# Kernel optimization log

Hardware: AMD Instinct MI355X
Metric: run time of the kernel (lower is better)

The kernel has to match this reference:

```python
import jax, jax.numpy as jnp
import numpy as np

B, S, D = 4, 2048, 512
H, DK, DV = 8, 64, 64
DFF = 2048
LN_EPS = 1e-5


def _layernorm(x, g, b):
    mu = jnp.mean(x, axis=-1, keepdims=True)
    var = jnp.mean(jnp.square(x - mu), axis=-1, keepdims=True)
    return (x - mu) * jax.lax.rsqrt(var + LN_EPS) * g + b


def setup_inputs() -> dict:
    key = jax.random.key(0)
    ks = jax.random.split(key, 9)
    def xavier(k, shape):
        fan_out, fan_in = shape
        std = np.sqrt(2.0 / (fan_in + fan_out))
        return jax.random.normal(k, shape, jnp.float32) * std
    GELU_GAIN = 1.85
    return {
        "x": jax.random.normal(ks[0], (B, S, D), jnp.float32),
        "attention_mask": jax.random.randint(ks[1], (B, S), 0, 2).astype(bool),
        "Wq": xavier(ks[2], (H * DK, D)),
        "Wk": xavier(ks[3], (H * DK, D)),
        "Wv": xavier(ks[4], (H * DV, D)),
        "Wp": xavier(ks[5], (D, H * DV)),
        "W1": xavier(ks[6], (DFF, D)) * GELU_GAIN,
        "b1": jnp.zeros((DFF,), jnp.float32),
        "W2": xavier(ks[7], (D, DFF)),
        "b2": jnp.zeros((D,), jnp.float32),
        "ln1_g": jnp.ones((D,), jnp.float32),
        "ln1_b": jnp.zeros((D,), jnp.float32),
        "ln2_g": jnp.ones((D,), jnp.float32),
        "ln2_b": jnp.zeros((D,), jnp.float32),
    }


def reference(x, attention_mask, Wq, Wk, Wv, Wp, W1, b1, W2, b2,
              ln1_g, ln1_b, ln2_g, ln2_b):
    b, s, d = x.shape
    residual = x
    q = (x @ Wq.T).reshape(b, s, H, DK)  # [B,S,H,DK]
    k = (x @ Wk.T).reshape(b, s, H, DK)
    v = (x @ Wv.T).reshape(b, s, H, DV)
    score = jnp.einsum("bshd,bthd->bhst", q, k) * (DK ** -0.5)  # [B,H,S,S]
    # subtractive mask: score -= 100 * not(mask)
    score = score - 100.0 * (~attention_mask)[:, None, None, :].astype(score.dtype)
    p = jax.nn.softmax(score, axis=-1)
    ctx = jnp.einsum("bhst,bthd->bshd", p, v).reshape(b, s, H * DV)
    att = ctx @ Wp.T  # dropout p=0.1 is identity in eval
    h = _layernorm(att + residual, ln1_g, ln1_b)
    ff = jax.nn.gelu(h @ W1.T + b1, approximate=False) @ W2.T + b2
    out = _layernorm(ff + h, ln2_g, ln2_b)
    return out
```

## Files before the change

### kernel.cpp

```cpp
#include <hip/hip_runtime.h>
#include <cstdint>
#include <cstddef>

#define B_ 4
#define S_ 2048
#define D_ 512
#define H_ 8
#define DK_ 64
#define DFF_ 2048

using s16x8  = __attribute__((ext_vector_type(8))) short;
using bf16x8 = __attribute__((ext_vector_type(8))) __bf16;
using f32x4  = __attribute__((ext_vector_type(4))) float;

__device__ __forceinline__ short f2bf(float f) {
  unsigned u = __builtin_bit_cast(unsigned, f);
  u += 0x7FFFu + ((u >> 16) & 1u);
  return (short)(u >> 16);
}
__device__ __forceinline__ float bf2f(short s) {
  unsigned u = ((unsigned)(unsigned short)s) << 16;
  return __builtin_bit_cast(float, u);
}

__device__ __forceinline__ void gl2lds16(const void* g, void* l) {
  __builtin_amdgcn_global_load_lds(
      (const __attribute__((address_space(1))) void*)g,
      (__attribute__((address_space(3))) void*)l, 16, 0, 0);
}

__global__ __launch_bounds__(256)
void cvt_all(const float* __restrict__ x, const float* __restrict__ Wq,
             const float* __restrict__ Wk, const float* __restrict__ Wv,
             const float* __restrict__ Wp, const float* __restrict__ W1,
             const float* __restrict__ W2,
             short* __restrict__ xb, short* __restrict__ wqkv,
             short* __restrict__ wp, short* __restrict__ w1, short* __restrict__ w2) {
  int blk = blockIdx.x;
  const float* src; short* dst; int off;
  if (blk < 4096)      { src = x;  dst = xb;            off = blk; }
  else if (blk < 4352) { src = Wq; dst = wqkv;          off = blk - 4096; }
  else if (blk < 4608) { src = Wk; dst = wqkv + 262144; off = blk - 4352; }
  else if (blk < 4864) { src = Wv; dst = wqkv + 524288; off = blk - 4608; }
  else if (blk < 5120) { src = Wp; dst = wp;            off = blk - 4864; }
  else if (blk < 6144) { src = W1; dst = w1;            off = blk - 5120; }
  else                 { src = W2; dst = w2;            off = blk - 6144; }
  int i = (off * 256 + threadIdx.x) * 4;
  float4 v = *(const float4*)(src + i);
  *(short4*)(dst + i) = make_short4(f2bf(v.x), f2bf(v.y), f2bf(v.z), f2bf(v.w));
}

template <int MODE>
__device__ __forceinline__ void gemm_store(int m0, int n, const f32x4& a,
                                           const float* __restrict__ aux1,
                                           void* out0, void* out1, void* out2,
                                           int M, int N) {
  if constexpr (MODE == 0) {
    const int bb = m0 >> 11, ss0 = m0 & 2047;
    if (n < 512) {
      short4 pk = make_short4(f2bf(a[0] * 0.18033688f), f2bf(a[1] * 0.18033688f),
                              f2bf(a[2] * 0.18033688f), f2bf(a[3] * 0.18033688f));
      *(short4*)((short*)out0 +
          ((((size_t)bb * H_ + (n >> 6)) * 64 + (n & 63)) * S_ + ss0)) = pk;
    } else if (n >= 1024) {
      const int nn = n - 1024;
      short4 pk = make_short4(f2bf(a[0]), f2bf(a[1]), f2bf(a[2]), f2bf(a[3]));
      *(short4*)((short*)out2 +
          ((((size_t)bb * H_ + (nn >> 6)) * 64 + (nn & 63)) * S_ + ss0)) = pk;
    } else {
      const int nn = n - 512;
      const size_t rowb = ((size_t)bb * H_ + (nn >> 6)) * S_ + ss0;
#pragma unroll
      for (int rr = 0; rr < 4; ++rr)
        ((short*)out1)[(rowb + rr) * 64 + (nn & 63)] = f2bf(a[rr]);
    }
  } else {
#pragma unroll
    for (int rr = 0; rr < 4; ++rr) {
      float t = a[rr] + aux1[n];
      float x2 = t * t;
      float t2 = t * (2.3022082f + 0.1029464f * x2);
      float e  = __builtin_amdgcn_exp2f(t2);
      float gl = t - t * __builtin_amdgcn_rcpf(1.0f + e);
      ((short*)out0)[(size_t)(m0 + rr) * N + n] = f2bf(gl);
    }
  }
}

__global__ __launch_bounds__(512)
void gemm_out_bf16(const short* __restrict__ A, const short* __restrict__ B,
                   int M, int N, int K, short* __restrict__ out) {
  __shared__ alignas(16) short As[2][128][64];
  __shared__ alignas(16) short Bs[2][128][64];

  const int tid  = threadIdx.x;
  const int lane = tid & 63;
  const int wave = tid >> 6;
  const int quad = lane >> 4;
  const int l16  = lane & 15;
  const int wm   = (wave >> 1) * 32;
  const int wn   = (wave & 1) * 64;
  const int bm   = blockIdx.x * 128;
  const int bn   = blockIdx.y * 128;

  const int srow8 = lane >> 3;
  const int pb    = lane & 7;

  f32x4 acc[2][4] = {};
  const int nt = K >> 6;

#pragma unroll
  for (int i = 0; i < 2; ++i) {
    const int rr = wave * 16 + i * 8 + srow8;
    const int cb = pb ^ (rr & 7);
    gl2lds16(A + (size_t)(bm + rr) * K + cb * 8, &As[0][wave * 16 + i * 8][0]);
    gl2lds16(B + (size_t)(bn + rr) * K + cb * 8, &Bs[0][wave * 16 + i * 8][0]);
  }
  __syncthreads();

  int cur = 0;
  for (int t = 0; t < nt; ++t) {
    if (t + 1 < nt) {
      const int kk = (t + 1) * 64;
#pragma unroll
      for (int i = 0; i < 2; ++i) {
        const int rr = wave * 16 + i * 8 + srow8;
        const int cb = pb ^ (rr & 7);
        gl2lds16(A + (size_t)(bm + rr) * K + kk + cb * 8, &As[cur ^ 1][wave * 16 + i * 8][0]);
        gl2lds16(B + (size_t)(bn + rr) * K + kk + cb * 8, &Bs[cur ^ 1][wave * 16 + i * 8][0]);
      }
    }

#pragma unroll
    for (int c = 0; c < 2; ++c) {
      bf16x8 a[2], b[4];
#pragma unroll
      for (int i = 0; i < 2; ++i) {
        const int row = wm + i * 16 + l16;
        a[i] = __builtin_bit_cast(bf16x8,
            *(const s16x8*)&As[cur][row][(((c * 4 + quad) ^ (row & 7))) * 8]);
      }
#pragma unroll
      for (int j = 0; j < 4; ++j) {
        const int row = wn + j * 16 + l16;
        b[j] = __builtin_bit_cast(bf16x8,
            *(const s16x8*)&Bs[cur][row][(((c * 4 + quad) ^ (row & 7))) * 8]);
      }
#pragma unroll
      for (int i = 0; i < 2; ++i)
#pragma unroll
        for (int j = 0; j < 4; ++j)
          acc[i][j] = __builtin_amdgcn_mfma_f32_16x16x32_bf16(a[i], b[j], acc[i][j], 0, 0, 0);
    }

    __syncthreads();
    cur ^= 1;
  }

#pragma unroll
  for (int i = 0; i < 2; ++i) {
    const int m0 = bm + wm + i * 16 + quad * 4;
#pragma unroll
    for (int j = 0; j < 4; ++j) {
      const int n = bn + wn + j * 16 + l16;
#pragma unroll
      for (int rr = 0; rr < 4; ++rr)
        out[(size_t)(m0 + rr) * N + n] = f2bf(acc[i][j][rr]);
    }
  }
}

template <int MODE>
__global__ __launch_bounds__(512)
void gemm256(const short* __restrict__ A, const short* __restrict__ B,
             int M, int N, int K,
             const float* __restrict__ aux1,
             void* __restrict__ out0, void* __restrict__ out1, void* __restrict__ out2) {
  __shared__ alignas(16) short As[2][256][64];
  __shared__ alignas(16) short Bs[2][256][64];

  const int tid  = threadIdx.x;
  const int lane = tid & 63;
  const int wave = tid >> 6;
  const int quad = lane >> 4;
  const int l16  = lane & 15;
  const int wm   = (wave >> 2) * 128;
  const int wn   = (wave & 3) * 64;
  const int bm   = blockIdx.x * 256;
  const int bn   = blockIdx.y * 256;

  const int srow8 = lane >> 3;
  const int pb    = lane & 7;

  f32x4 acc[8][4] = {};
  const int nt = K >> 6;

#pragma unroll
  for (int p = 0; p < 4; ++p) {
    const int rr = p * 64 + wave * 8 + srow8;
    const int cb = pb ^ (rr & 7);
    gl2lds16(A + (size_t)(bm + rr) * K + cb * 8, &As[0][p * 64 + wave * 8][0]);
    gl2lds16(B + (size_t)(bn + rr) * K + cb * 8, &Bs[0][p * 64 + wave * 8][0]);
  }
  __syncthreads();

  int cur = 0;
  for (int t = 0; t < nt; ++t) {
    if (t + 1 < nt) {
      const int kk = (t + 1) * 64;
#pragma unroll
      for (int p = 0; p < 4; ++p) {
        const int rr = p * 64 + wave * 8 + srow8;
        const int cb = pb ^ (rr & 7);
        gl2lds16(A + (size_t)(bm + rr) * K + kk + cb * 8, &As[cur ^ 1][p * 64 + wave * 8][0]);
        gl2lds16(B + (size_t)(bn + rr) * K + kk + cb * 8, &Bs[cur ^ 1][p * 64 + wave * 8][0]);
      }
    }

#pragma unroll
    for (int c = 0; c < 2; ++c) {
      bf16x8 a[8], b[4];
#pragma unroll
      for (int i = 0; i < 8; ++i) {
        const int row = wm + i * 16 + l16;
        a[i] = __builtin_bit_cast(bf16x8,
            *(const s16x8*)&As[cur][row][(((c * 4 + quad) ^ (row & 7))) * 8]);
      }
#pragma unroll
      for (int j = 0; j < 4; ++j) {
        const int row = wn + j * 16 + l16;
        b[j] = __builtin_bit_cast(bf16x8,
            *(const s16x8*)&Bs[cur][row][(((c * 4 + quad) ^ (row & 7))) * 8]);
      }
#pragma unroll
      for (int i = 0; i < 8; ++i)
#pragma unroll
        for (int j = 0; j < 4; ++j)
          acc[i][j] = __builtin_amdgcn_mfma_f32_16x16x32_bf16(a[i], b[j], acc[i][j], 0, 0, 0);
    }

    __syncthreads();
    cur ^= 1;
  }

#pragma unroll
  for (int i = 0; i < 8; ++i) {
    const int m0 = bm + wm + i * 16 + quad * 4;
#pragma unroll
    for (int j = 0; j < 4; ++j)
      gemm_store<MODE>(m0, bn + wn + j * 16 + l16, acc[i][j], aux1,
                       out0, out1, out2, M, N);
  }
}

__global__ __launch_bounds__(512)
void flash_attn_mfma(const short* __restrict__ QTg, const short* __restrict__ Kb,
                     const short* __restrict__ Vtg, const void* __restrict__ mraw,
                     short* __restrict__ ctxb) {
  __shared__ alignas(16) short Ks[64][64];
  __shared__ alignas(16) short Vt[64][64];
  __shared__ alignas(16) short Ps[8][32][64];
  __shared__ alignas(8) unsigned char mbits8[256];
  __shared__ unsigned red[8];

  int flat = (blockIdx.z * 8 + blockIdx.y) * 8 + blockIdx.x;
  flat = (flat & 7) * 32 + (flat >> 3);
  const int b = flat >> 6, h = (flat >> 3) & 7;
  const int q0 = (flat & 7) * 256;

  const int tid = threadIdx.x;
  const int w = tid >> 6, lane = tid & 63;
  const int quad = lane >> 4, l16 = lane & 15;
  const size_t base  = ((size_t)(b * H_ + h)) * S_ * DK_;
  const size_t baseT = ((size_t)(b * H_ + h)) * DK_ * S_;

  {
    const unsigned* mw = (const unsigned*)mraw;
    unsigned v = 0;
#pragma unroll
    for (int i = 0; i < 4; ++i) v |= mw[tid + i * 512];
#pragma unroll
    for (int s = 1; s < 64; s <<= 1) v |= __shfl_xor(v, s);
    if (lane == 0) red[w] = v;
    __syncthreads();
    unsigned f = red[0] | red[1] | red[2] | red[3] |
                 red[4] | red[5] | red[6] | red[7];
    if (tid < 256) {
      unsigned byte = 0;
#pragma unroll
      for (int j = 0; j < 8; ++j) {
        int t = tid * 8 + j;
        int gidx = b * S_ + t;
        int val;
        if ((f & ~1u) == 0u)            val = ((const int*)mraw)[gidx];
        else if (f == 0x3F800000u)      val = (((const float*)mraw)[gidx] != 0.0f);
        else                            val = ((const unsigned char*)mraw)[gidx];
        byte |= (val ? 1u : 0u) << j;
      }
      mbits8[tid] = (unsigned char)byte;
    }
  }

  bf16x8 qa[2][2];
#pragma unroll
  for (int st = 0; st < 2; ++st) {
    const int q = q0 + w * 32 + st * 16 + l16;
#pragma unroll
    for (int c = 0; c < 2; ++c) {
      s16x8 t;
#pragma unroll
      for (int j = 0; j < 8; ++j)
        t[j] = QTg[baseT + (size_t)(c * 32 + quad * 8 + j) * S_ + q];
      qa[st][c] = __builtin_bit_cast(bf16x8, t);
    }
  }

  f32x4 Oc[2][4] = {};
  float li[2] = {};
  const int swz = l16 & 7;

  const int r = tid >> 3, cc = tid & 7;
  const short* kp = Kb  + base  + (size_t)r * 64 + cc * 8;
  const short* vp = Vtg + baseT + (size_t)r * S_ + cc * 8;
  const int ch = ((cc ^ (r & 7)) << 3);

  s16x8 kr = *(const s16x8*)(kp);
  s16x8 vr = *(const s16x8*)(vp);

  for (int t0 = 0; t0 < S_; t0 += 64) {
    __syncthreads();
    *(s16x8*)&Ks[r][ch] = kr;
    *(s16x8*)&Vt[r][ch] = vr;
    __syncthreads();

    if (t0 + 64 < S_) {
      kr = *(const s16x8*)(kp + (size_t)(t0 + 64) * 64);
      vr = *(const s16x8*)(vp + (t0 + 64));
    }

    f32x4 sc[2][4] = {};
    __builtin_amdgcn_s_setprio(1);
#pragma unroll
    for (int c = 0; c < 2; ++c) {
#pragma unroll
      for (int jt = 0; jt < 4; ++jt) {
        bf16x8 kb = __builtin_bit_cast(bf16x8,
            *(const s16x8*)&Ks[jt * 16 + l16][((c * 4 + quad) ^ swz) << 3]);
        sc[0][jt] = __builtin_amdgcn_mfma_f32_16x16x32_bf16(kb, qa[0][c], sc[0][jt], 0, 0, 0);
        sc[1][jt] = __builtin_amdgcn_mfma_f32_16x16x32_bf16(kb, qa[1][c], sc[1][jt], 0, 0, 0);
      }
    }
    __builtin_amdgcn_s_setprio(0);

    const unsigned long long mball =
        *(const unsigned long long*)&mbits8[t0 >> 3];
#pragma unroll
    for (int jt = 0; jt < 4; ++jt) {
      const unsigned m16 = ((unsigned)(mball >> (jt * 16))) >> (quad * 4);
      const int pch = (((jt * 2 + (quad >> 1)) ^ swz) << 3) + (quad & 1) * 4;
#pragma unroll
      for (int st = 0; st < 2; ++st) {
        unsigned uu[4];
#pragma unroll
        for (int rr = 0; rr < 4; ++rr) {
          float pe = __builtin_amdgcn_exp2f(sc[st][jt][rr]);
          unsigned u = __builtin_bit_cast(unsigned, pe) & 0xFFFF0000u;
          u = ((m16 >> rr) & 1u) ? u : 0u;
          li[st] += __builtin_bit_cast(float, u);
          uu[rr] = u;
        }
        *(uint2*)&Ps[w][st * 16 + l16][pch] =
            make_uint2(__builtin_amdgcn_perm(uu[1], uu[0], 0x07060302u),
                       __builtin_amdgcn_perm(uu[3], uu[2], 0x07060302u));
      }
    }

    __builtin_amdgcn_s_setprio(1);
#pragma unroll
    for (int c = 0; c < 2; ++c) {
      bf16x8 pa0 = __builtin_bit_cast(bf16x8,
          *(const s16x8*)&Ps[w][l16][((c * 4 + quad) ^ swz) << 3]);
      bf16x8 pa1 = __builtin_bit_cast(bf16x8,
          *(const s16x8*)&Ps[w][16 + l16][((c * 4 + quad) ^ swz) << 3]);
#pragma unroll
      for (int dt = 0; dt < 4; ++dt) {
        bf16x8 vb = __builtin_bit_cast(bf16x8,
            *(const s16x8*)&Vt[dt * 16 + l16][((c * 4 + quad) ^ swz) << 3]);
        Oc[0][dt] = __builtin_amdgcn_mfma_f32_16x16x32_bf16(pa0, vb, Oc[0][dt], 0, 0, 0);
        Oc[1][dt] = __builtin_amdgcn_mfma_f32_16x16x32_bf16(pa1, vb, Oc[1][dt], 0, 0, 0);
      }
    }
    __builtin_amdgcn_s_setprio(0);
  }

#pragma unroll
  for (int st = 0; st < 2; ++st) {
    float l = li[st];
    l += __shfl_xor(l, 16);
    l += __shfl_xor(l, 32);
#pragma unroll
    for (int rr = 0; rr < 4; ++rr) {
      float lr = __shfl(l, quad * 4 + rr);
      float inv = 1.f / lr;
      const size_t row = (size_t)b * S_ + q0 + w * 32 + st * 16 + quad * 4 + rr;
#pragma unroll
      for (int dt = 0; dt < 4; ++dt)
        ctxb[row * (H_ * DK_) + h * 64 + dt * 16 + l16] = f2bf(Oc[st][dt][rr] * inv);
    }
  }
}

__global__ __launch_bounds__(256)
void ln_fused(const float* __restrict__ p0, const float* __restrict__ p1,
              const float* __restrict__ xres, const short* __restrict__ hres,
              const short* __restrict__ hres2,
              const float* __restrict__ bias,
              const float* __restrict__ g, const float* __restrict__ bb,
              float* __restrict__ out32, short* __restrict__ outb) {
  const int wave = threadIdx.x >> 6, lane = threadIdx.x & 63;
  const int token = blockIdx.x * 4 + wave;
  const size_t off = (size_t)token * D_;
  const int c = lane * 8;

  float v[8] = {0.f, 0.f, 0.f, 0.f, 0.f, 0.f, 0.f, 0.f};
  if (p0) {
    float4 a0 = *(const float4*)(p0 + off + c);
    float4 a1 = *(const float4*)(p0 + off + c + 4);
    float4 b0 = *(const float4*)(p1 + off + c);
    float4 b1 = *(const float4*)(p1 + off + c + 4);
    v[0]+=a0.x+b0.x; v[1]+=a0.y+b0.y; v[2]+=a0.z+b0.z; v[3]+=a0.w+b0.w;
    v[4]+=a1.x+b1.x; v[5]+=a1.y+b1.y; v[6]+=a1.z+b1.z; v[7]+=a1.w+b1.w;
  }
  if (xres) {
    float4 x0 = *(const float4*)(xres + off + c);
    float4 x1 = *(const float4*)(xres + off + c + 4);
    v[0]+=x0.x; v[1]+=x0.y; v[2]+=x0.z; v[3]+=x0.w;
    v[4]+=x1.x; v[5]+=x1.y; v[6]+=x1.z; v[7]+=x1.w;
  }
  if (hres) {
    short4 h0 = *(const short4*)(hres + off + c);
    short4 h1 = *(const short4*)(hres + off + c + 4);
    v[0]+=bf2f(h0.x); v[1]+=bf2f(h0.y); v[2]+=bf2f(h0.z); v[3]+=bf2f(h0.w);
    v[4]+=bf2f(h1.x); v[5]+=bf2f(h1.y); v[6]+=bf2f(h1.z); v[7]+=bf2f(h1.w);
  }
  if (hres2) {
    short4 h0 = *(const short4*)(hres2 + off + c);
    short4 h1 = *(const short4*)(hres2 + off + c + 4);
    v[0]+=bf2f(h0.x); v[1]+=bf2f(h0.y); v[2]+=bf2f(h0.z); v[3]+=bf2f(h0.w);
    v[4]+=bf2f(h1.x); v[5]+=bf2f(h1.y); v[6]+=bf2f(h1.z); v[7]+=bf2f(h1.w);
  }
  if (bias) {
    float4 c0 = *(const float4*)(bias + c);
    float4 c1 = *(const float4*)(bias + c + 4);
    v[0]+=c0.x; v[1]+=c0.y; v[2]+=c0.z; v[3]+=c0.w;
    v[4]+=c1.x; v[5]+=c1.y; v[6]+=c1.z; v[7]+=c1.w;
  }

  float sum = 0.f;
#pragma unroll
  for (int i = 0; i < 8; ++i) sum += v[i];
#pragma unroll
  for (int m = 1; m < 64; m <<= 1) sum += __shfl_xor(sum, m);
  float mu = sum * (1.0f / D_);
  float vs = 0.f;
#pragma unroll
  for (int i = 0; i < 8; ++i) { v[i] -= mu; vs += v[i] * v[i]; }
#pragma unroll
  for (int m = 1; m < 64; m <<= 1) vs += __shfl_xor(vs, m);
  float rstd = rsqrtf(vs * (1.0f / D_) + 1e-5f);
#pragma unroll
  for (int i = 0; i < 8; ++i) {
    float val = v[i] * rstd * g[c + i] + bb[c + i];
    if (out32) out32[off + c + i] = val;
    if (outb)  outb[off + c + i] = f2bf(val);
  }
}

constexpr size_t OFF_XB   = 0;
constexpr size_t OFF_WQKV = 8388608;
constexpr size_t OFF_WP   = 9961472;
constexpr size_t OFF_W1   = 10485760;
constexpr size_t OFF_W2   = 12582912;
constexpr size_t OFF_QT   = 14680064;
constexpr size_t OFF_K    = 23068672;
constexpr size_t OFF_VT   = 31457280;
constexpr size_t OFF_CTX  = 39845888;
constexpr size_t OFF_ATT  = 48234496;
constexpr size_t OFF_FF2  = 65011712;
constexpr size_t OFF_HB   = 81788928;
constexpr size_t OFF_FF1  = 14680064;
constexpr size_t WS_NEED  = 90177536;

extern "C" void kernel_launch(void* const* d_in, const int* in_sizes, int n_in,
                              void* d_out, int out_size, void* d_ws, size_t ws_size,
                              hipStream_t stream) {
  if (ws_size < WS_NEED) return;

  const float* x    = (const float*)d_in[0];
  const void*  msk  = d_in[1];
  const float* Wq   = (const float*)d_in[2];
  const float* Wk   = (const float*)d_in[3];
  const float* Wv   = (const float*)d_in[4];
  const float* Wp   = (const float*)d_in[5];
  const float* W1   = (const float*)d_in[6];
  const float* b1   = (const float*)d_in[7];
  const float* W2   = (const float*)d_in[8];
  const float* b2   = (const float*)d_in[9];
  const float* ln1g = (const float*)d_in[10];
  const float* ln1b = (const float*)d_in[11];
  const float* ln2g = (const float*)d_in[12];
  const float* ln2b = (const float*)d_in[13];

  char* ws = (char*)d_ws;
  short* xb    = (short*)(ws + OFF_XB);
  short* wqkv  = (short*)(ws + OFF_WQKV);
  short* Wpb   = (short*)(ws + OFF_WP);
  short* W1b   = (short*)(ws + OFF_W1);
  short* W2b   = (short*)(ws + OFF_W2);
  short* QTb   = (short*)(ws + OFF_QT);
  short* Kbh   = (short*)(ws + OFF_K);
  short* VTb   = (short*)(ws + OFF_VT);
  short* ctxb  = (short*)(ws + OFF_CTX);
  short* attb  = (short*)(ws + OFF_ATT);
  short* ff2b  = (short*)(ws + OFF_FF2);
  short* hb    = (short*)(ws + OFF_HB);
  short* ff1b  = (short*)(ws + OFF_FF1);

  cvt_all<<<7168, 256, 0, stream>>>(x, Wq, Wk, Wv, Wp, W1, W2,
                                    xb, wqkv, Wpb, W1b, W2b);

  gemm256<0><<<dim3(32, 6, 1), 512, 0, stream>>>(xb, wqkv, 8192, 1536, 512,
                                                 nullptr, QTb, Kbh, VTb);

  flash_attn_mfma<<<dim3(S_ / 256, H_, B_), 512, 0, stream>>>(QTb, Kbh, VTb, msk, ctxb);

  gemm_out_bf16<<<dim3(64, 4, 1), 512, 0, stream>>>(ctxb, Wpb, 8192, 512, 512, attb);

  ln_fused<<<2048, 256, 0, stream>>>(nullptr, nullptr, x, attb, nullptr, nullptr,
                                     ln1g, ln1b, nullptr, hb);

  gemm256<2><<<dim3(32, 8, 1), 512, 0, stream>>>(hb, W1b, 8192, 2048, 512,
                                                 b1, ff1b, nullptr, nullptr);

  gemm_out_bf16<<<dim3(64, 4, 1), 512, 0, stream>>>(ff1b, W2b, 8192, 512, 2048, ff2b);

  ln_fused<<<2048, 256, 0, stream>>>(nullptr, nullptr, nullptr, hb, ff2b, b2,
                                     ln2g, ln2b, (float*)d_out, nullptr);
}
```

Before: 283.1 us.

## Switch flash attention to 32x32x16 MFMA and keep P in registers

The attention kernel moves from 16x16x32 MFMA tiles to 32x32x16 tiles for both QK^T and PV. The probability matrix is no longer staged through a per-wave LDS buffer: it is packed to bf16 with v_cvt_pk_bf16_f32 and rearranged across lanes with v_permlane32_swap to form the A operand directly. This removes LDS writes and reads of P and reduces the number of MFMA issues. The cost is larger accumulator vectors and more register pressure. P now uses round-to-nearest bf16 conversion, while the row sum li is accumulated from the unrounded fp32 values, so the normalisation differs slightly from before.

```diff
diff --git a/kernel.cpp b/kernel.cpp
--- a/kernel.cpp
+++ b/kernel.cpp
@@ -12,6 +12,7 @@
 using s16x8  = __attribute__((ext_vector_type(8))) short;
 using bf16x8 = __attribute__((ext_vector_type(8))) __bf16;
 using f32x4  = __attribute__((ext_vector_type(4))) float;
+using f32x16 = __attribute__((ext_vector_type(16))) float;
 
 __device__ __forceinline__ short f2bf(float f) {
   unsigned u = __builtin_bit_cast(unsigned, f);
@@ -21,6 +22,15 @@
 __device__ __forceinline__ float bf2f(short s) {
   unsigned u = ((unsigned)(unsigned short)s) << 16;
   return __builtin_bit_cast(float, u);
+}
+
+__device__ __forceinline__ unsigned cvtpk(float a, float b) {
+  unsigned r;
+  asm("v_cvt_pk_bf16_f32 %0, %1, %2" : "=v"(r) : "v"(a), "v"(b));
+  return r;
+}
+__device__ __forceinline__ void pl32swap(unsigned& a, unsigned& b) {
+  asm("v_permlane32_swap_b32 %0, %1" : "+v"(a), "+v"(b));
 }
 
 __device__ __forceinline__ void gl2lds16(const void* g, void* l) {
@@ -259,7 +269,6 @@
                      short* __restrict__ ctxb) {
   __shared__ alignas(16) short Ks[64][64];
   __shared__ alignas(16) short Vt[64][64];
-  __shared__ alignas(16) short Ps[8][32][64];
   __shared__ alignas(8) unsigned char mbits8[256];
   __shared__ unsigned red[8];
 
@@ -270,7 +279,7 @@
 
   const int tid = threadIdx.x;
   const int w = tid >> 6, lane = tid & 63;
-  const int quad = lane >> 4, l16 = lane & 15;
+  const int l32 = lane & 31, hi = lane >> 5;
   const size_t base  = ((size_t)(b * H_ + h)) * S_ * DK_;
   const size_t baseT = ((size_t)(b * H_ + h)) * DK_ * S_;
 
@@ -301,23 +310,22 @@
     }
   }
 
-  bf16x8 qa[2][2];
-#pragma unroll
-  for (int st = 0; st < 2; ++st) {
-    const int q = q0 + w * 32 + st * 16 + l16;
-#pragma unroll
-    for (int c = 0; c < 2; ++c) {
+  bf16x8 qa[4];
+  {
+    const int q = q0 + w * 32 + l32;
+#pragma unroll
+    for (int s4 = 0; s4 < 4; ++s4) {
       s16x8 t;
 #pragma unroll
       for (int j = 0; j < 8; ++j)
-        t[j] = QTg[baseT + (size_t)(c * 32 + quad * 8 + j) * S_ + q];
-      qa[st][c] = __builtin_bit_cast(bf16x8, t);
-    }
-  }
-
-  f32x4 Oc[2][4] = {};
-  float li[2] = {};
-  const int swz = l16 & 7;
+        t[j] = QTg[baseT + (size_t)(s4 * 16 + hi * 8 + j) * S_ + q];
+      qa[s4] = __builtin_bit_cast(bf16x8, t);
+    }
+  }
+
+  f32x16 Oc[2] = {};
+  float li = 0.f;
+  const int swzkey = l32 & 7;
 
   const int r = tid >> 3, cc = tid & 7;
   const short* kp = Kb  + base  + (size_t)r * 64 + cc * 8;
@@ -338,76 +346,77 @@
       vr = *(const s16x8*)(vp + (t0 + 64));
     }
 
-    f32x4 sc[2][4] = {};
+    f32x16 sc0 = {}, sc1 = {};
     __builtin_amdgcn_s_setprio(1);
 #pragma unroll
-    for (int c = 0; c < 2; ++c) {
-#pragma unroll
-      for (int jt = 0; jt < 4; ++jt) {
-        bf16x8 kb = __builtin_bit_cast(bf16x8,
-            *(const s16x8*)&Ks[jt * 16 + l16][((c * 4 + quad) ^ swz) << 3]);
-        sc[0][jt] = __builtin_amdgcn_mfma_f32_16x16x32_bf16(kb, qa[0][c], sc[0][jt], 0, 0, 0);
-        sc[1][jt] = __builtin_amdgcn_mfma_f32_16x16x32_bf16(kb, qa[1][c], sc[1][jt], 0, 0, 0);
-      }
+    for (int s4 = 0; s4 < 4; ++s4) {
+      const int chn = ((s4 * 2 + hi) ^ swzkey) << 3;
+      bf16x8 kb0 = __builtin_bit_cast(bf16x8, *(const s16x8*)&Ks[l32][chn]);
+      bf16x8 kb1 = __builtin_bit_cast(bf16x8, *(const s16x8*)&Ks[32 + l32][chn]);
+      sc0 = __builtin_amdgcn_mfma_f32_32x32x16_bf16(kb0, qa[s4], sc0, 0, 0, 0);
+      sc1 = __builtin_amdgcn_mfma_f32_32x32x16_bf16(kb1, qa[s4], sc1, 0, 0, 0);
     }
     __builtin_amdgcn_s_setprio(0);
 
     const unsigned long long mball =
         *(const unsigned long long*)&mbits8[t0 >> 3];
-#pragma unroll
-    for (int jt = 0; jt < 4; ++jt) {
-      const unsigned m16 = ((unsigned)(mball >> (jt * 16))) >> (quad * 4);
-      const int pch = (((jt * 2 + (quad >> 1)) ^ swz) << 3) + (quad & 1) * 4;
-#pragma unroll
-      for (int st = 0; st < 2; ++st) {
-        unsigned uu[4];
-#pragma unroll
-        for (int rr = 0; rr < 4; ++rr) {
-          float pe = __builtin_amdgcn_exp2f(sc[st][jt][rr]);
-          unsigned u = __builtin_bit_cast(unsigned, pe) & 0xFFFF0000u;
-          u = ((m16 >> rr) & 1u) ? u : 0u;
-          li[st] += __builtin_bit_cast(float, u);
-          uu[rr] = u;
-        }
-        *(uint2*)&Ps[w][st * 16 + l16][pch] =
-            make_uint2(__builtin_amdgcn_perm(uu[1], uu[0], 0x07060302u),
-                       __builtin_amdgcn_perm(uu[3], uu[2], 0x07060302u));
+    float pA[16], pB[16];
+#pragma unroll
+    for (int rg = 0; rg < 4; ++rg) {
+      const unsigned mA = (unsigned)(mball >> (rg * 8 + hi * 4)) & 15u;
+      const unsigned mB = (unsigned)(mball >> (32 + rg * 8 + hi * 4)) & 15u;
+#pragma unroll
+      for (int rr = 0; rr < 4; ++rr) {
+        const int reg = rg * 4 + rr;
+        float eA = __builtin_amdgcn_exp2f(sc0[reg]);
+        float eB = __builtin_amdgcn_exp2f(sc1[reg]);
+        pA[reg] = ((mA >> rr) & 1u) ? eA : 0.f;
+        pB[reg] = ((mB >> rr) & 1u) ? eB : 0.f;
+        li += pA[reg] + pB[reg];
       }
     }
 
     __builtin_amdgcn_s_setprio(1);
-#pragma unroll
-    for (int c = 0; c < 2; ++c) {
-      bf16x8 pa0 = __builtin_bit_cast(bf16x8,
-          *(const s16x8*)&Ps[w][l16][((c * 4 + quad) ^ swz) << 3]);
-      bf16x8 pa1 = __builtin_bit_cast(bf16x8,
-          *(const s16x8*)&Ps[w][16 + l16][((c * 4 + quad) ^ swz) << 3]);
-#pragma unroll
-      for (int dt = 0; dt < 4; ++dt) {
-        bf16x8 vb = __builtin_bit_cast(bf16x8,
-            *(const s16x8*)&Vt[dt * 16 + l16][((c * 4 + quad) ^ swz) << 3]);
-        Oc[0][dt] = __builtin_amdgcn_mfma_f32_16x16x32_bf16(pa0, vb, Oc[0][dt], 0, 0, 0);
-        Oc[1][dt] = __builtin_amdgcn_mfma_f32_16x16x32_bf16(pa1, vb, Oc[1][dt], 0, 0, 0);
-      }
-    }
+#define PVSTEP(S4, PS, BB)                                                    \
+    {                                                                         \
+      unsigned w0 = cvtpk(PS[BB + 0], PS[BB + 1]);                            \
+      unsigned w1 = cvtpk(PS[BB + 2], PS[BB + 3]);                            \
+      unsigned w2 = cvtpk(PS[BB + 4], PS[BB + 5]);                            \
+      unsigned w3 = cvtpk(PS[BB + 6], PS[BB + 7]);                            \
+      pl32swap(w0, w2);                                                       \
+      pl32swap(w1, w3);                                                       \
+      uint4 pw = make_uint4(w0, w1, w2, w3);                                  \
+      bf16x8 pa = __builtin_bit_cast(bf16x8, pw);                             \
+      const int chn = (((S4) * 2 + hi) ^ swzkey) << 3;                        \
+      bf16x8 vb0 = __builtin_bit_cast(bf16x8, *(const s16x8*)&Vt[l32][chn]);  \
+      bf16x8 vb1 = __builtin_bit_cast(bf16x8, *(const s16x8*)&Vt[32 + l32][chn]); \
+      Oc[0] = __builtin_amdgcn_mfma_f32_32x32x16_bf16(pa, vb0, Oc[0], 0, 0, 0);   \
+      Oc[1] = __builtin_amdgcn_mfma_f32_32x32x16_bf16(pa, vb1, Oc[1], 0, 0, 0);   \
+    }
+    PVSTEP(0, pA, 0)
+    PVSTEP(1, pA, 8)
+    PVSTEP(2, pB, 0)
+    PVSTEP(3, pB, 8)
+#undef PVSTEP
     __builtin_amdgcn_s_setprio(0);
   }
 
-#pragma unroll
-  for (int st = 0; st < 2; ++st) {
-    float l = li[st];
-    l += __shfl_xor(l, 16);
-    l += __shfl_xor(l, 32);
-#pragma unroll
-    for (int rr = 0; rr < 4; ++rr) {
-      float lr = __shfl(l, quad * 4 + rr);
-      float inv = 1.f / lr;
-      const size_t row = (size_t)b * S_ + q0 + w * 32 + st * 16 + quad * 4 + rr;
-#pragma unroll
-      for (int dt = 0; dt < 4; ++dt)
-        ctxb[row * (H_ * DK_) + h * 64 + dt * 16 + l16] = f2bf(Oc[st][dt][rr] * inv);
-    }
-  }
+  li += __shfl_xor(li, 32);
+  float inv[16];
+#pragma unroll
+  for (int reg = 0; reg < 16; ++reg) {
+    const int qq = (reg & 3) + 8 * (reg >> 2) + 4 * hi;
+    inv[reg] = 1.f / __shfl(li, qq);
+  }
+  const size_t rowbase = (size_t)b * S_ + q0 + w * 32;
+#pragma unroll
+  for (int dt = 0; dt < 2; ++dt)
+#pragma unroll
+    for (int reg = 0; reg < 16; ++reg) {
+      const int qq = (reg & 3) + 8 * (reg >> 2) + 4 * hi;
+      ctxb[(rowbase + qq) * (H_ * DK_) + h * 64 + dt * 32 + l32] =
+          f2bf(Oc[dt][reg] * inv[reg]);
+    }
 }
 
 __global__ __launch_bounds__(256)
```

Result: no change. 285.7 us (+0.9%).
